# Kernel tuning notes

Measured on AMD Instinct MI355X. Metric: run time of the kernel, lower is better.

Reference implementation:

```python
import jax, jax.numpy as jnp
import numpy as np

B, S, H = 2, 2048, 2048
NH, HD = 16, 128
I = 8192
EPS = float(np.finfo(np.float32).eps)  # torch RMSNorm default eps=None -> dtype eps


def rmsnorm(x, w):
    var = jnp.mean(jnp.square(x), axis=-1, keepdims=True)
    return x * jax.lax.rsqrt(var + EPS) * w


def setup_inputs() -> dict:
    key = jax.random.key(0)
    ks = jax.random.split(key, 8)
    s = 0.02
    return {
        "hidden_states": jax.random.normal(ks[0], (B, S, H), jnp.float32),
        "Wq": jax.random.normal(ks[1], (H, H), jnp.float32) * s,
        "Wk": jax.random.normal(ks[2], (H, H), jnp.float32) * s,
        "Wv": jax.random.normal(ks[3], (H, H), jnp.float32) * s,
        "Wo": jax.random.normal(ks[4], (H, H), jnp.float32) * s,
        "Wg": jax.random.normal(ks[5], (I, H), jnp.float32) * s,
        "Wu": jax.random.normal(ks[6], (I, H), jnp.float32) * s,
        "Wd": jax.random.normal(ks[7], (H, I), jnp.float32) * s,
        "g_in": jnp.ones((H,), jnp.float32),
        "g_post": jnp.ones((H,), jnp.float32),
    }


def reference(hidden_states, Wq, Wk, Wv, Wo, Wg, Wu, Wd, g_in, g_post):
    residual = hidden_states
    x = rmsnorm(hidden_states, g_in)
    # projections: nn.Linear does x @ W.T
    q = (x @ Wq.T).reshape(B, S, NH, HD).transpose(0, 2, 1, 3)  # [B,NH,S,HD]
    k = (x @ Wk.T).reshape(B, S, NH, HD).transpose(0, 2, 1, 3)
    v = (x @ Wv.T).reshape(B, S, NH, HD).transpose(0, 2, 1, 3)
    scores = jnp.einsum("bhqd,bhkd->bhqk", q, k) / jnp.sqrt(jnp.float32(HD))
    attn = jax.nn.softmax(scores, axis=-1)
    out = jnp.einsum("bhqk,bhkd->bhqd", attn, v)
    out = out.transpose(0, 2, 1, 3).reshape(B, S, H)
    hidden_states = residual + out @ Wo.T
    residual = hidden_states
    x = rmsnorm(hidden_states, g_post)
    mlp = (jax.nn.silu(x @ Wg.T) * (x @ Wu.T)) @ Wd.T
    return residual + mlp
```

## Files before the change

### kernel.cpp

```cpp
#include <hip/hip_runtime.h>

using u16 = unsigned short;
using u32 = unsigned int;

typedef __attribute__((ext_vector_type(8))) __bf16 bf16x8;
typedef __attribute__((ext_vector_type(4))) float f32x4;

__device__ __forceinline__ u16 f2bf(float f) {
  __bf16 h = (__bf16)f;
  return __builtin_bit_cast(u16, h);
}
__device__ __forceinline__ u32 pk2(float a, float b) {
  return (u32)f2bf(a) | ((u32)f2bf(b) << 16);
}
__device__ __forceinline__ float bf2f(u16 h) {
  return __uint_as_float(((u32)h) << 16);
}
__device__ __forceinline__ void gload16(const u16* g, u16* l) {
  __builtin_amdgcn_global_load_lds((const __attribute__((address_space(1))) void*)g,
                                   (__attribute__((address_space(3))) void*)l, 16, 0, 0);
}
__device__ __forceinline__ f32x4 mfma_bf16(bf16x8 a, bf16x8 b, f32x4 c) {
  return __builtin_amdgcn_mfma_f32_16x16x32_bf16(a, b, c, 0, 0, 0);
}

__global__ __launch_bounds__(256) void cvt_bf16(const float* __restrict__ in,
                                                u16* __restrict__ out, int n8) {
  int i = blockIdx.x * 256 + threadIdx.x;
  int stride = gridDim.x * 256;
  for (; i < n8; i += stride) {
    float4 a = ((const float4*)in)[(size_t)i * 2];
    float4 b = ((const float4*)in)[(size_t)i * 2 + 1];
    ((uint4*)out)[i] = make_uint4(pk2(a.x, a.y), pk2(a.z, a.w), pk2(b.x, b.y), pk2(b.z, b.w));
  }
}

struct CvtJobs {
  const float* in[7];
  u16* out[7];
  int n8[7];
};
__global__ __launch_bounds__(256) void cvt_all(CvtJobs c) {
  const int stride = gridDim.x * 256;
  const int base = blockIdx.x * 256 + threadIdx.x;
#pragma unroll
  for (int j = 0; j < 7; ++j) {
    const float* in = c.in[j];
    u16* out = c.out[j];
    const int n8 = c.n8[j];
    for (int i = base; i < n8; i += stride) {
      float4 a = ((const float4*)in)[(size_t)i * 2];
      float4 b = ((const float4*)in)[(size_t)i * 2 + 1];
      ((uint4*)out)[i] = make_uint4(pk2(a.x, a.y), pk2(a.z, a.w), pk2(b.x, b.y), pk2(b.z, b.w));
    }
  }
}

__global__ __launch_bounds__(256) void rmsnorm_bf16(const float* __restrict__ x,
                                                    const float* __restrict__ g,
                                                    u16* __restrict__ o) {
  const int row = blockIdx.x;
  const int tid = threadIdx.x;
  const float4* xr = (const float4*)(x + (size_t)row * 2048);
  float4 a = xr[tid * 2], b = xr[tid * 2 + 1];
  float s = a.x * a.x + a.y * a.y + a.z * a.z + a.w * a.w +
            b.x * b.x + b.y * b.y + b.z * b.z + b.w * b.w;
#pragma unroll
  for (int off = 1; off < 64; off <<= 1) s += __shfl_xor(s, off);
  __shared__ float red[4];
  if ((tid & 63) == 0) red[tid >> 6] = s;
  __syncthreads();
  s = red[0] + red[1] + red[2] + red[3];
  const float r = rsqrtf(s * (1.0f / 2048.0f) + 1.1920929e-07f);
  const float4* gr = (const float4*)g;
  float4 ga = gr[tid * 2], gb = gr[tid * 2 + 1];
  ((uint4*)(o + (size_t)row * 2048))[tid] =
      make_uint4(pk2(a.x * r * ga.x, a.y * r * ga.y), pk2(a.z * r * ga.z, a.w * r * ga.w),
                 pk2(b.x * r * gb.x, b.y * r * gb.y), pk2(b.z * r * gb.z, b.w * r * gb.w));
}

__global__ __launch_bounds__(512, 2) void gemmGU(const u16* __restrict__ A,
                                                 const u16* __restrict__ Bg,
                                                 const u16* __restrict__ Bu,
                                                 u16* __restrict__ Out,
                                                 int M, int N, int K) {
  alignas(16) __shared__ u16 lds[2 * 32768];
  const int tid = threadIdx.x;
  const int w = tid >> 6, lane = tid & 63;
  const int lo = lane & 15, hi = lane >> 4;
  const int nbm = M >> 8, nbx = N >> 7;
  const int RM = nbm >> 1, RN = nbx >> 2;
  const int xcd = blockIdx.x & 7, bidx = blockIdx.x >> 3;
  const int bm = ((xcd >> 2) * RM + bidx / RN) << 8;
  const int bn = ((xcd & 3) * RN + bidx % RN) << 7;
  const int wm = w >> 1, wn = w & 1;

  const int rw = (hi ^ ((lo >> 1) & 3)) * 8;
  const int arow0 = wm * 64 + lo, brow0 = wn * 64 + lo;

  const int srow = tid >> 2;
  const int scol = ((tid & 3) ^ ((tid >> 3) & 3)) * 8;
  const u16* Ab = A + (size_t)(bm + srow) * K + scol;
  const u16* Bgb = Bg + (size_t)(bn + srow) * K + scol;
  const u16* Bub = Bu + (size_t)(bn + srow) * K + scol;

  f32x4 gacc[4][4] = {}, uacc[4][4] = {};
  bf16x8 af[4], bf[4];

#define AOFF(par, kh) ((par)*32768 + (kh)*8192)
#define BGOFF(par, kh) ((par)*32768 + 16384 + (kh)*4096)
#define BUOFF(par, kh) ((par)*32768 + 24576 + (kh)*4096)
#define STG_A(par, kh, kt)                                                  \
  {                                                                         \
    gload16(Ab + (kt) + (kh)*32, &lds[AOFF(par, kh) + tid * 8]);            \
    gload16(Ab + (size_t)128 * K + (kt) + (kh)*32,                          \
            &lds[AOFF(par, kh) + 4096 + tid * 8]);                          \
  }
#define STG_B(par, kh, kt)                                                  \
  {                                                                         \
    gload16(Bgb + (kt) + (kh)*32, &lds[BGOFF(par, kh) + tid * 8]);          \
    gload16(Bub + (kt) + (kh)*32, &lds[BUOFF(par, kh) + tid * 8]);          \
  }
#define PHASE_SYNC()                                   \
  __builtin_amdgcn_s_barrier();                        \
  asm volatile("s_waitcnt lgkmcnt(0)" ::: "memory");   \
  __builtin_amdgcn_sched_barrier(0);
#define MFMA16(ACC)                                                         \
  __builtin_amdgcn_s_setprio(1);                                            \
  _Pragma("unroll") for (int m_ = 0; m_ < 4; ++m_)                          \
      _Pragma("unroll") for (int n_ = 0; n_ < 4; ++n_)                      \
          ACC[m_][n_] = mfma_bf16(af[m_], bf[n_], ACC[m_][n_]);             \
  __builtin_amdgcn_s_setprio(0);

  STG_A(0, 0, 0); STG_B(0, 0, 0); STG_A(0, 1, 0); STG_B(0, 1, 0);
  asm volatile("s_waitcnt vmcnt(0)" ::: "memory");
  __builtin_amdgcn_s_barrier();

  const int NT = K >> 6;
  for (int t = 0; t < NT; ++t) {
    const int par = t & 1, np = par ^ 1;
    const int ktn = (t + 1) << 6;
    const bool pre = (t + 1 < NT);

#pragma unroll
    for (int n = 0; n < 4; ++n)
      bf[n] = *(const bf16x8*)(&lds[BGOFF(par, 0)] + (brow0 + n * 16) * 32 + rw);
#pragma unroll
    for (int m = 0; m < 4; ++m)
      af[m] = *(const bf16x8*)(&lds[AOFF(par, 0)] + (arow0 + m * 16) * 32 + rw);
    if (pre) STG_A(np, 0, ktn);
    PHASE_SYNC();
    MFMA16(gacc);

#pragma unroll
    for (int n = 0; n < 4; ++n)
      bf[n] = *(const bf16x8*)(&lds[BUOFF(par, 0)] + (brow0 + n * 16) * 32 + rw);
    if (pre) STG_B(np, 0, ktn);
    if (pre) { asm volatile("s_waitcnt vmcnt(4)" ::: "memory"); }
    else     { asm volatile("s_waitcnt vmcnt(0)" ::: "memory"); }
    PHASE_SYNC();
    MFMA16(uacc);

#pragma unroll
    for (int n = 0; n < 4; ++n)
      bf[n] = *(const bf16x8*)(&lds[BGOFF(par, 1)] + (brow0 + n * 16) * 32 + rw);
#pragma unroll
    for (int m = 0; m < 4; ++m)
      af[m] = *(const bf16x8*)(&lds[AOFF(par, 1)] + (arow0 + m * 16) * 32 + rw);
    if (pre) STG_A(np, 1, ktn);
    PHASE_SYNC();
    MFMA16(gacc);

#pragma unroll
    for (int n = 0; n < 4; ++n)
      bf[n] = *(const bf16x8*)(&lds[BUOFF(par, 1)] + (brow0 + n * 16) * 32 + rw);
    if (pre) STG_B(np, 1, ktn);
    if (pre) { asm volatile("s_waitcnt vmcnt(4)" ::: "memory"); }
    PHASE_SYNC();
    MFMA16(uacc);
  }
#undef AOFF
#undef BGOFF
#undef BUOFF
#undef STG_A
#undef STG_B
#undef PHASE_SYNC
#undef MFMA16

#pragma unroll
  for (int m = 0; m < 4; ++m) {
    const int gr = bm + wm * 64 + m * 16 + hi * 4;
#pragma unroll
    for (int n = 0; n < 4; ++n) {
      const int gc = bn + wn * 64 + n * 16 + lo;
#pragma unroll
      for (int r = 0; r < 4; ++r) {
        float g = gacc[m][n][r];
        float s = g / (1.f + __expf(-g));
        Out[(size_t)(gr + r) * N + gc] = f2bf(s * uacc[m][n][r]);
      }
    }
  }
}

template <int EPI>
__global__ __launch_bounds__(512, 1) void gemm3b(const u16* __restrict__ A,
                                                 const u16* __restrict__ B,
                                                 u16* Cb, float* Cf,
                                                 const float* __restrict__ Res,
                                                 int M, int N, int K, int lda) {
  constexpr int BUF = 24576;
  alignas(16) __shared__ u16 lds[3 * BUF];
  const int tid = threadIdx.x;
  const int w = tid >> 6, lane = tid & 63;
  const int lo = lane & 15, hi = lane >> 4;

  const int nbm = M >> 8, nbx = N >> 7;
  const int RM = nbm >> 1, RN = nbx >> 2;
  const int xcd = blockIdx.x & 7, idx = blockIdx.x >> 3;
  const int bm = ((xcd >> 2) * RM + idx / RN) << 8;
  const int bn = ((xcd & 3) * RN + idx % RN) << 7;

  const int wm = w >> 1, wn = w & 1;
  const int scol = ((tid & 7) ^ ((tid >> 3) & 7)) * 8;
  const u16* Ag = A + (size_t)(bm + (tid >> 3)) * lda + scol;
  const u16* Bg = B + (size_t)(bn + (tid >> 3)) * K + scol;

  f32x4 acc[4][4] = {};

#define STG(b, kt)                                                                    \
  {                                                                                   \
    _Pragma("unroll") for (int c = 0; c < 4; ++c)                                     \
        gload16(Ag + (size_t)(c * 64) * lda + (kt), &lds[(b)*BUF + c * 4096 + tid * 8]); \
    _Pragma("unroll") for (int c = 0; c < 2; ++c)                                     \
        gload16(Bg + (size_t)(c * 64) * K + (kt), &lds[(b)*BUF + 16384 + c * 4096 + tid * 8]); \
  }

  const int NT = K >> 6;
  STG(0, 0);
  STG(1, 64);

  int cur = 0;
  for (int T = 0; T < NT; ++T) {
    if (T + 1 < NT) {
      asm volatile("s_waitcnt vmcnt(6)" ::: "memory");
    } else {
      asm volatile("s_waitcnt vmcnt(0)" ::: "memory");
    }
    __builtin_amdgcn_s_barrier();
    __builtin_amdgcn_sched_barrier(0);

    const u16* LA = &lds[cur * BUF];
    const u16* LB = LA + 16384;
    bf16x8 af[4][2], bf[4][2];
#pragma unroll
    for (int ks = 0; ks < 2; ++ks) {
#pragma unroll
      for (int m = 0; m < 4; ++m)
        af[m][ks] = *(const bf16x8*)(LA + (wm * 64 + m * 16 + lo) * 64 +
                                     ((ks * 4 + hi) ^ (lo & 7)) * 8);
#pragma unroll
      for (int n = 0; n < 4; ++n)
        bf[n][ks] = *(const bf16x8*)(LB + (wn * 64 + n * 16 + lo) * 64 +
                                     ((ks * 4 + hi) ^ (lo & 7)) * 8);
    }
    if (T + 2 < NT) {
      const int nb = (cur + 2) % 3;
      STG(nb, (T + 2) << 6);
    }
    __builtin_amdgcn_s_setprio(1);
#pragma unroll
    for (int ks = 0; ks < 2; ++ks)
#pragma unroll
      for (int m = 0; m < 4; ++m)
#pragma unroll
        for (int n = 0; n < 4; ++n) acc[m][n] = mfma_bf16(af[m][ks], bf[n][ks], acc[m][n]);
    __builtin_amdgcn_s_setprio(0);
    cur = (cur + 1) % 3;
  }
#undef STG

#pragma unroll
  for (int m = 0; m < 4; ++m) {
    const int gr = bm + wm * 64 + m * 16 + hi * 4;
#pragma unroll
    for (int n = 0; n < 4; ++n) {
      const int gc = bn + wn * 64 + n * 16 + lo;
#pragma unroll
      for (int r = 0; r < 4; ++r) {
        const size_t idx2 = (size_t)(gr + r) * N + gc;
        if constexpr (EPI == 1) {
          Cf[idx2] = Res[idx2] + acc[m][n][r];
        } else if constexpr (EPI == 2) {
          float g = bf2f(Cb[idx2]);
          float s = g / (1.f + __expf(-g));
          Cb[idx2] = f2bf(s * acc[m][n][r]);
        } else {
          Cb[idx2] = f2bf(acc[m][n][r]);
        }
      }
    }
  }
}

template <int EPI>
__global__ __launch_bounds__(256) void gemm_bt(const u16* __restrict__ A,
                                               const float* __restrict__ B,
                                               u16* Cb, float* Cf, const float* Res,
                                               int M, int N, int K) {
  alignas(16) __shared__ u16 As[128 * 32];
  alignas(16) __shared__ u16 Bs[128 * 32];
  const int tid = threadIdx.x;
  const int w = tid >> 6, lane = tid & 63;
  const int lo = lane & 15, hi = lane >> 4;
  const int bm = blockIdx.y * 128, bn = blockIdx.x * 128;
  const int wr = (w >> 1) * 64, wc = (w & 1) * 64;
  f32x4 acc[4][4] = {};
  const int r0 = tid >> 2, kc0 = (tid & 3) * 8;
  const u16* a0 = A + (size_t)(bm + r0) * K + kc0;
  const u16* a1 = A + (size_t)(bm + 64 + r0) * K + kc0;
  const float* b0 = B + (size_t)(bn + r0) * K + kc0;
  const float* b1 = B + (size_t)(bn + 64 + r0) * K + kc0;
  u16* asd0 = &As[(size_t)tid * 8];
  u16* asd1 = &As[(size_t)(tid + 256) * 8];
  u16* bsd0 = &Bs[(size_t)tid * 8];
  u16* bsd1 = &Bs[(size_t)(tid + 256) * 8];
  for (int kt = 0; kt < K; kt += 32) {
    gload16(a0 + kt, asd0);
    gload16(a1 + kt, asd1);
    float4 x0 = *(const float4*)(b0 + kt);
    float4 x1 = *(const float4*)(b0 + kt + 4);
    float4 y0 = *(const float4*)(b1 + kt);
    float4 y1 = *(const float4*)(b1 + kt + 4);
    *(uint4*)bsd0 = make_uint4(pk2(x0.x, x0.y), pk2(x0.z, x0.w), pk2(x1.x, x1.y), pk2(x1.z, x1.w));
    *(uint4*)bsd1 = make_uint4(pk2(y0.x, y0.y), pk2(y0.z, y0.w), pk2(y1.x, y1.y), pk2(y1.z, y1.w));
    __syncthreads();
    bf16x8 af[4], bfr[4];
#pragma unroll
    for (int i = 0; i < 4; ++i) {
      af[i] = *(const bf16x8*)(&As[(wr + i * 16 + lo) * 32 + hi * 8]);
      bfr[i] = *(const bf16x8*)(&Bs[(wc + i * 16 + lo) * 32 + hi * 8]);
    }
#pragma unroll
    for (int i = 0; i < 4; ++i)
#pragma unroll
      for (int j = 0; j < 4; ++j) acc[i][j] = mfma_bf16(af[i], bfr[j], acc[i][j]);
    __syncthreads();
  }
#pragma unroll
  for (int i = 0; i < 4; ++i) {
    const int gr = bm + wr + i * 16 + hi * 4;
#pragma unroll
    for (int j = 0; j < 4; ++j) {
      const int gc = bn + wc + j * 16 + lo;
#pragma unroll
      for (int r = 0; r < 4; ++r) {
        const size_t idx = (size_t)(gr + r) * N + gc;
        if constexpr (EPI == 1) {
          Cf[idx] = Res[idx] + acc[i][j][r];
        } else if constexpr (EPI == 2) {
          float g = bf2f(Cb[idx]);
          float s = g / (1.f + __expf(-g));
          Cb[idx] = f2bf(s * acc[i][j][r]);
        } else {
          Cb[idx] = f2bf(acc[i][j][r]);
        }
      }
    }
  }
}

__global__ __launch_bounds__(256) void transpose_v(const u16* __restrict__ v,
                                                   u16* __restrict__ vt, int ldv) {
  __shared__ u16 t[32][33];
  const int bh = blockIdx.z, b = bh >> 4, h = bh & 15;
  const int s0 = blockIdx.x * 32, d0 = blockIdx.y * 32;
  const int tx = threadIdx.x, ty = threadIdx.y;
#pragma unroll
  for (int i = 0; i < 4; ++i)
    t[ty + i * 8][tx] = v[(size_t)(b * 2048 + s0 + ty + i * 8) * ldv + h * 128 + d0 + tx];
  __syncthreads();
#pragma unroll
  for (int i = 0; i < 4; ++i)
    vt[(size_t)(bh * 128 + d0 + ty + i * 8) * 2048 + s0 + tx] = t[tx][ty + i * 8];
}

__global__ __launch_bounds__(512) void attn_fwd3(const u16* __restrict__ q,
                                                 const u16* __restrict__ k,
                                                 const u16* __restrict__ vt,
                                                 u16* o, int ldq) {
  constexpr int S = 2048;
  alignas(16) __shared__ u16 Ks[2][64 * 128];
  alignas(16) __shared__ u16 Vs[2][128 * 64];
  alignas(16) __shared__ u16 plds[8][16 * 68];
  const int bh = blockIdx.y, b = bh >> 4, h = bh & 15;
  const int tid = threadIdx.x, w = tid >> 6, lane = tid & 63;
  const int lo = lane & 15, hi = lane >> 4;
  const int qr = blockIdx.x * 128 + w * 16;
  u16* pl = &plds[w][0];

  bf16x8 qf[4];
  const u16* qb = q + (size_t)(b * S + qr + lo) * ldq + h * 128 + hi * 8;
#pragma unroll
  for (int ks = 0; ks < 4; ++ks) qf[ks] = *(const bf16x8*)(qb + ks * 32);

  f32x4 oacc[8] = {};
  f32x4 lp = {0.f, 0.f, 0.f, 0.f};

  const u16* kb = k + (size_t)(b * S) * ldq + h * 128;
  const u16* vb = vt + (size_t)bh * 128 * S;

  const int kcs = ((tid & 15) ^ ((tid >> 4) & 7)) * 8;
  const int vcs = ((tid & 7) ^ ((tid >> 3) & 7)) * 8;
  const u16* kgs = kb + (size_t)(tid >> 4) * ldq + kcs;
  const u16* vgs = vb + (size_t)(tid >> 3) * S + vcs;

  int cur = 0;
#pragma unroll
  for (int c = 0; c < 2; ++c) gload16(kgs + (size_t)(c * 32) * ldq, &Ks[0][c * 4096 + tid * 8]);
#pragma unroll
  for (int c = 0; c < 2; ++c) gload16(vgs + (size_t)(c * 64) * S, &Vs[0][c * 4096 + tid * 8]);
  __syncthreads();

  const int swq = (lo & 7) << 4;
  constexpr float SCL = 0.12752956f;

  for (int kv = 0; kv < S; kv += 64) {
    if (kv + 64 < S) {
      const int nb = cur ^ 1;
#pragma unroll
      for (int c = 0; c < 2; ++c)
        gload16(kgs + (size_t)(kv + 64 + c * 32) * ldq, &Ks[nb][c * 4096 + tid * 8]);
#pragma unroll
      for (int c = 0; c < 2; ++c)
        gload16(vgs + (size_t)(c * 64) * S + kv + 64, &Vs[nb][c * 4096 + tid * 8]);
    }
    const u16* Kc = &Ks[cur][0];
    const u16* Vc = &Vs[cur][0];

    f32x4 sacc[4] = {};
    __builtin_amdgcn_s_setprio(1);
#pragma unroll
    for (int ks = 0; ks < 4; ++ks)
#pragma unroll
      for (int n = 0; n < 4; ++n) {
        bf16x8 kf = *(const bf16x8*)(Kc + (n * 16 + lo) * 128 + (((ks * 64 + hi * 16) ^ swq) >> 1));
        sacc[n] = mfma_bf16(qf[ks], kf, sacc[n]);
      }
    __builtin_amdgcn_s_setprio(0);

    f32x4 p[4];
#pragma unroll
    for (int n = 0; n < 4; ++n)
#pragma unroll
      for (int r = 0; r < 4; ++r) p[n][r] = exp2f(sacc[n][r] * SCL);
#pragma unroll
    for (int r = 0; r < 4; ++r)
      lp[r] += (p[0][r] + p[1][r]) + (p[2][r] + p[3][r]);

#pragma unroll
    for (int n = 0; n < 4; ++n)
#pragma unroll
      for (int r = 0; r < 4; ++r)
        pl[(hi * 4 + r) * 68 + n * 16 + lo] = f2bf(p[n][r]);
    asm volatile("s_waitcnt lgkmcnt(0)" ::: "memory");
    bf16x8 pf0 = *(const bf16x8*)(pl + lo * 68 + hi * 8);
    bf16x8 pf1 = *(const bf16x8*)(pl + lo * 68 + 32 + hi * 8);

    __builtin_amdgcn_s_setprio(1);
#pragma unroll
    for (int f = 0; f < 8; ++f) {
      const int row = f * 16 + lo;
      bf16x8 vf0 = *(const bf16x8*)(Vc + row * 64 + (((hi * 16) ^ swq) >> 1));
      bf16x8 vf1 = *(const bf16x8*)(Vc + row * 64 + (((64 + hi * 16) ^ swq) >> 1));
      oacc[f] = mfma_bf16(pf0, vf0, oacc[f]);
      oacc[f] = mfma_bf16(pf1, vf1, oacc[f]);
    }
    __builtin_amdgcn_s_setprio(0);

    __syncthreads();
    cur ^= 1;
  }

  float l[4];
#pragma unroll
  for (int r = 0; r < 4; ++r) l[r] = lp[r];
#pragma unroll
  for (int off = 1; off < 16; off <<= 1)
#pragma unroll
    for (int r = 0; r < 4; ++r) l[r] += __shfl_xor(l[r], off);

  u16* ob = o + (size_t)(b * S + qr) * ldq + h * 128;
#pragma unroll
  for (int f = 0; f < 8; ++f)
#pragma unroll
    for (int r = 0; r < 4; ++r)
      ob[(size_t)(hi * 4 + r) * ldq + f * 16 + lo] = f2bf(oacc[f][r] / l[r]);
}

extern "C" void kernel_launch(void* const* d_in, const int* in_sizes, int n_in,
                              void* d_out, int out_size, void* d_ws, size_t ws_size,
                              hipStream_t stream) {
  constexpr int B = 2, S = 2048, H = 2048, NH = 16, I = 8192;
  constexpr int M = B * S;

  const float* hs = (const float*)d_in[0];
  const float* Wq = (const float*)d_in[1];
  const float* Wk = (const float*)d_in[2];
  const float* Wv = (const float*)d_in[3];
  const float* Wo = (const float*)d_in[4];
  const float* Wg = (const float*)d_in[5];
  const float* Wu = (const float*)d_in[6];
  const float* Wd = (const float*)d_in[7];
  const float* g_in = (const float*)d_in[8];
  const float* g_post = (const float*)d_in[9];
  float* out = (float*)d_out;

  constexpr size_t SZ_HH = (size_t)H * H * 2;
  constexpr size_t SZ_IH = (size_t)I * H * 2;
  constexpr size_t SZ_MH = (size_t)M * H * 2;
  constexpr size_t NEED_ALL = 5 * SZ_MH + 3 * SZ_HH + SZ_HH + 3 * SZ_IH;
  constexpr size_t NEED_FUSED = SZ_MH + 3 * SZ_MH + SZ_MH + 2 * SZ_IH;
  constexpr size_t NEED_BASE = SZ_MH + 3 * SZ_MH + SZ_MH + SZ_IH;

  if (ws_size >= NEED_ALL) {
    char* p = (char*)d_ws;
    u16* x_b = (u16*)p;    p += SZ_MH;
    u16* qkv_b = (u16*)p;  p += 3 * SZ_MH;
    u16* vt_b = (u16*)p;   p += SZ_MH;
    u16* wqkv = (u16*)p;   p += 3 * SZ_HH;
    u16* wo_b = (u16*)p;   p += SZ_HH;
    u16* wg_b = (u16*)p;   p += SZ_IH;
    u16* wu_b = (u16*)p;   p += SZ_IH;
    u16* wd_b = (u16*)p;   p += SZ_IH;
    u16* gate_b = qkv_b;

    rmsnorm_bf16<<<M, 256, 0, stream>>>(hs, g_in, x_b);

    CvtJobs cj;
    cj.in[0] = Wq;  cj.out[0] = wqkv;                     cj.n8[0] = H * H / 8;
    cj.in[1] = Wk;  cj.out[1] = wqkv + (size_t)H * H;     cj.n8[1] = H * H / 8;
    cj.in[2] = Wv;  cj.out[2] = wqkv + (size_t)2 * H * H; cj.n8[2] = H * H / 8;
    cj.in[3] = Wo;  cj.out[3] = wo_b;                     cj.n8[3] = H * H / 8;
    cj.in[4] = Wg;  cj.out[4] = wg_b;                     cj.n8[4] = I * H / 8;
    cj.in[5] = Wu;  cj.out[5] = wu_b;                     cj.n8[5] = I * H / 8;
    cj.in[6] = Wd;  cj.out[6] = wd_b;                     cj.n8[6] = I * H / 8;
    cvt_all<<<2048, 256, 0, stream>>>(cj);

    gemm3b<0><<<(M / 256) * (3 * H / 128), 512, 0, stream>>>(
        x_b, wqkv, qkv_b, nullptr, nullptr, M, 3 * H, H, H);

    transpose_v<<<dim3(S / 32, 128 / 32, B * NH), dim3(32, 8), 0, stream>>>(
        qkv_b + 2 * H, vt_b, 3 * H);
    attn_fwd3<<<dim3(S / 128, B * NH), 512, 0, stream>>>(qkv_b, qkv_b + H, vt_b, qkv_b, 3 * H);

    gemm3b<1><<<(M / 256) * (H / 128), 512, 0, stream>>>(
        qkv_b, wo_b, nullptr, out, hs, M, H, H, 3 * H);

    rmsnorm_bf16<<<M, 256, 0, stream>>>(out, g_post, x_b);

    gemmGU<<<(M / 256) * (I / 128), 512, 0, stream>>>(x_b, wg_b, wu_b, gate_b, M, I, H);

    gemm3b<1><<<(M / 256) * (H / 128), 512, 0, stream>>>(
        gate_b, wd_b, nullptr, out, out, M, H, I, I);
    return;
  }

  if (ws_size >= NEED_BASE) {
    char* p = (char*)d_ws;
    u16* x_b = (u16*)p;    p += SZ_MH;
    u16* qkv_b = (u16*)p;  p += 3 * SZ_MH;
    u16* vt_b = (u16*)p;   p += SZ_MH;
    u16* wsc = (u16*)p;    p += SZ_IH;
    u16* gate_b = qkv_b;
    const bool fused = ws_size >= NEED_FUSED;
    u16* wu_b = fused ? (u16*)p : nullptr;

    rmsnorm_bf16<<<M, 256, 0, stream>>>(hs, g_in, x_b);

    cvt_bf16<<<1024, 256, 0, stream>>>(Wq, wsc, H * H / 8);
    cvt_bf16<<<1024, 256, 0, stream>>>(Wk, wsc + (size_t)H * H, H * H / 8);
    cvt_bf16<<<1024, 256, 0, stream>>>(Wv, wsc + (size_t)2 * H * H, H * H / 8);
    gemm3b<0><<<(M / 256) * (3 * H / 128), 512, 0, stream>>>(
        x_b, wsc, qkv_b, nullptr, nullptr, M, 3 * H, H, H);

    transpose_v<<<dim3(S / 32, 128 / 32, B * NH), dim3(32, 8), 0, stream>>>(
        qkv_b + 2 * H, vt_b, 3 * H);
    attn_fwd3<<<dim3(S / 128, B * NH), 512, 0, stream>>>(qkv_b, qkv_b + H, vt_b, qkv_b, 3 * H);

    cvt_bf16<<<1024, 256, 0, stream>>>(Wo, wsc, H * H / 8);
    gemm3b<1><<<(M / 256) * (H / 128), 512, 0, stream>>>(
        qkv_b, wsc, nullptr, out, hs, M, H, H, 3 * H);

    rmsnorm_bf16<<<M, 256, 0, stream>>>(out, g_post, x_b);

    if (fused) {
      cvt_bf16<<<1024, 256, 0, stream>>>(Wg, wsc, I * H / 8);
      cvt_bf16<<<1024, 256, 0, stream>>>(Wu, wu_b, I * H / 8);
      gemmGU<<<(M / 256) * (I / 128), 512, 0, stream>>>(x_b, wsc, wu_b, gate_b, M, I, H);
    } else {
      cvt_bf16<<<1024, 256, 0, stream>>>(Wg, wsc, I * H / 8);
      gemm3b<0><<<(M / 256) * (I / 128), 512, 0, stream>>>(
          x_b, wsc, gate_b, nullptr, nullptr, M, I, H, H);
      cvt_bf16<<<1024, 256, 0, stream>>>(Wu, wsc, I * H / 8);
      gemm3b<2><<<(M / 256) * (I / 128), 512, 0, stream>>>(
          x_b, wsc, gate_b, nullptr, nullptr, M, I, H, H);
    }
    cvt_bf16<<<1024, 256, 0, stream>>>(Wd, wsc, I * H / 8);
    gemm3b<1><<<(M / 256) * (H / 128), 512, 0, stream>>>(
        gate_b, wsc, nullptr, out, out, M, H, I, I);
    return;
  }

  constexpr int MC = 2048;
  char* p = (char*)d_ws;
  u16* x_b = (u16*)p;   p += SZ_MH;
  u16* q_b = (u16*)p;   p += SZ_MH;
  u16* k_b = (u16*)p;   p += SZ_MH;
  u16* v_b = (u16*)p;   p += SZ_MH;
  u16* vt_b = (u16*)p;  p += SZ_MH;
  u16* g_mlp = k_b;

  rmsnorm_bf16<<<M, 256, 0, stream>>>(hs, g_in, x_b);
  const dim3 gHH(H / 128, M / 128);
  gemm_bt<0><<<gHH, 256, 0, stream>>>(x_b, Wq, q_b, nullptr, nullptr, M, H, H);
  gemm_bt<0><<<gHH, 256, 0, stream>>>(x_b, Wk, k_b, nullptr, nullptr, M, H, H);
  gemm_bt<0><<<gHH, 256, 0, stream>>>(x_b, Wv, v_b, nullptr, nullptr, M, H, H);
  transpose_v<<<dim3(S / 32, 128 / 32, B * NH), dim3(32, 8), 0, stream>>>(v_b, vt_b, H);
  attn_fwd3<<<dim3(S / 128, B * NH), 512, 0, stream>>>(q_b, k_b, vt_b, q_b, H);
  gemm_bt<1><<<gHH, 256, 0, stream>>>(q_b, Wo, nullptr, out, hs, M, H, H);
  rmsnorm_bf16<<<M, 256, 0, stream>>>(out, g_post, x_b);
  const dim3 gIH(I / 128, MC / 128), gHI(H / 128, MC / 128);
  for (int mc = 0; mc < M / MC; ++mc) {
    const u16* xc = x_b + (size_t)mc * MC * H;
    float* oc = out + (size_t)mc * MC * H;
    gemm_bt<0><<<gIH, 256, 0, stream>>>(xc, Wg, g_mlp, nullptr, nullptr, MC, I, H);
    gemm_bt<2><<<gIH, 256, 0, stream>>>(xc, Wu, g_mlp, nullptr, nullptr, MC, I, H);
    gemm_bt<1><<<gHI, 256, 0, stream>>>(g_mlp, Wd, nullptr, oc, oc, MC, H, I);
  }
}
```

Measured before the change: 782.7 us.

## Switch gemmGU and gemm3b to 32x32x16 bf16 MFMA tiles

Replaces the 16x16x32 MFMA instruction with the 32x32x16 variant in the fused gate/up GEMM and the generic triple-buffered GEMM. Each wave now covers its 64x64 tile as a 2x2 grid of 32x32 blocks, with new swizzled LDS fragment addressing and remapped epilogue rows. This is meant to cut the LDS fragment reads per MFMA and the instruction count while raising arithmetic intensity per register fragment. gemmGU's launch bound drops from 2 blocks to 1 block per CU, which loosens the register cap but may lower occupancy.

```diff
diff --git a/kernel.cpp b/kernel.cpp
--- a/kernel.cpp
+++ b/kernel.cpp
@@ -5,6 +5,7 @@
 
 typedef __attribute__((ext_vector_type(8))) __bf16 bf16x8;
 typedef __attribute__((ext_vector_type(4))) float f32x4;
+typedef __attribute__((ext_vector_type(16))) float f32x16;
 
 __device__ __forceinline__ u16 f2bf(float f) {
   __bf16 h = (__bf16)f;
@@ -22,6 +23,9 @@
 }
 __device__ __forceinline__ f32x4 mfma_bf16(bf16x8 a, bf16x8 b, f32x4 c) {
   return __builtin_amdgcn_mfma_f32_16x16x32_bf16(a, b, c, 0, 0, 0);
+}
+__device__ __forceinline__ f32x16 mfma32(bf16x8 a, bf16x8 b, f32x16 c) {
+  return __builtin_amdgcn_mfma_f32_32x32x16_bf16(a, b, c, 0, 0, 0);
 }
 
 __global__ __launch_bounds__(256) void cvt_bf16(const float* __restrict__ in,
@@ -79,7 +83,7 @@
                  pk2(b.x * r * gb.x, b.y * r * gb.y), pk2(b.z * r * gb.z, b.w * r * gb.w));
 }
 
-__global__ __launch_bounds__(512, 2) void gemmGU(const u16* __restrict__ A,
+__global__ __launch_bounds__(512, 1) void gemmGU(const u16* __restrict__ A,
                                                  const u16* __restrict__ Bg,
                                                  const u16* __restrict__ Bu,
                                                  u16* __restrict__ Out,
@@ -87,7 +91,7 @@
   alignas(16) __shared__ u16 lds[2 * 32768];
   const int tid = threadIdx.x;
   const int w = tid >> 6, lane = tid & 63;
-  const int lo = lane & 15, hi = lane >> 4;
+  const int l31 = lane & 31, lh = lane >> 5;
   const int nbm = M >> 8, nbx = N >> 7;
   const int RM = nbm >> 1, RN = nbx >> 2;
   const int xcd = blockIdx.x & 7, bidx = blockIdx.x >> 3;
@@ -95,8 +99,10 @@
   const int bn = ((xcd & 3) * RN + bidx % RN) << 7;
   const int wm = w >> 1, wn = w & 1;
 
-  const int rw = (hi ^ ((lo >> 1) & 3)) * 8;
-  const int arow0 = wm * 64 + lo, brow0 = wn * 64 + lo;
+  const int keyA = (l31 >> 1) & 3;
+  const int aw0 = ((lh ^ keyA)) * 8;
+  const int arow = (wm * 64 + l31) * 32;
+  const int brow = (wn * 64 + l31) * 32;
 
   const int srow = tid >> 2;
   const int scol = ((tid & 3) ^ ((tid >> 3) & 3)) * 8;
@@ -104,8 +110,8 @@
   const u16* Bgb = Bg + (size_t)(bn + srow) * K + scol;
   const u16* Bub = Bu + (size_t)(bn + srow) * K + scol;
 
-  f32x4 gacc[4][4] = {}, uacc[4][4] = {};
-  bf16x8 af[4], bf[4];
+  f32x16 gacc[2][2] = {}, uacc[2][2] = {};
+  bf16x8 af[2][2], bf[2][2];
 
 #define AOFF(par, kh) ((par)*32768 + (kh)*8192)
 #define BGOFF(par, kh) ((par)*32768 + 16384 + (kh)*4096)
@@ -125,11 +131,22 @@
   __builtin_amdgcn_s_barrier();                        \
   asm volatile("s_waitcnt lgkmcnt(0)" ::: "memory");   \
   __builtin_amdgcn_sched_barrier(0);
-#define MFMA16(ACC)                                                         \
-  __builtin_amdgcn_s_setprio(1);                                            \
-  _Pragma("unroll") for (int m_ = 0; m_ < 4; ++m_)                          \
-      _Pragma("unroll") for (int n_ = 0; n_ < 4; ++n_)                      \
-          ACC[m_][n_] = mfma_bf16(af[m_], bf[n_], ACC[m_][n_]);             \
+#define LD_A(slot)                                                             \
+  _Pragma("unroll") for (int mb = 0; mb < 2; ++mb)                             \
+      _Pragma("unroll") for (int kq = 0; kq < 2; ++kq)                         \
+          af[mb][kq] = *(const bf16x8*)(&lds[(slot) + arow + mb * 1024 +       \
+                                             (aw0 ^ (kq * 16))]);
+#define LD_B(slot)                                                             \
+  _Pragma("unroll") for (int nb = 0; nb < 2; ++nb)                             \
+      _Pragma("unroll") for (int kq = 0; kq < 2; ++kq)                         \
+          bf[nb][kq] = *(const bf16x8*)(&lds[(slot) + brow + nb * 1024 +       \
+                                             (aw0 ^ (kq * 16))]);
+#define MFMA8(ACC)                                                             \
+  __builtin_amdgcn_s_setprio(1);                                               \
+  _Pragma("unroll") for (int kq = 0; kq < 2; ++kq)                             \
+      _Pragma("unroll") for (int mb = 0; mb < 2; ++mb)                         \
+          _Pragma("unroll") for (int nb = 0; nb < 2; ++nb)                     \
+              ACC[mb][nb] = mfma32(af[mb][kq], bf[nb][kq], ACC[mb][nb]);       \
   __builtin_amdgcn_s_setprio(0);
 
   STG_A(0, 0, 0); STG_B(0, 0, 0); STG_A(0, 1, 0); STG_B(0, 1, 0);
@@ -142,42 +159,30 @@
     const int ktn = (t + 1) << 6;
     const bool pre = (t + 1 < NT);
 
-#pragma unroll
-    for (int n = 0; n < 4; ++n)
-      bf[n] = *(const bf16x8*)(&lds[BGOFF(par, 0)] + (brow0 + n * 16) * 32 + rw);
-#pragma unroll
-    for (int m = 0; m < 4; ++m)
-      af[m] = *(const bf16x8*)(&lds[AOFF(par, 0)] + (arow0 + m * 16) * 32 + rw);
+    LD_B(BGOFF(par, 0));
+    LD_A(AOFF(par, 0));
     if (pre) STG_A(np, 0, ktn);
     PHASE_SYNC();
-    MFMA16(gacc);
-
-#pragma unroll
-    for (int n = 0; n < 4; ++n)
-      bf[n] = *(const bf16x8*)(&lds[BUOFF(par, 0)] + (brow0 + n * 16) * 32 + rw);
+    MFMA8(gacc);
+
+    LD_B(BUOFF(par, 0));
     if (pre) STG_B(np, 0, ktn);
     if (pre) { asm volatile("s_waitcnt vmcnt(4)" ::: "memory"); }
     else     { asm volatile("s_waitcnt vmcnt(0)" ::: "memory"); }
     PHASE_SYNC();
-    MFMA16(uacc);
-
-#pragma unroll
-    for (int n = 0; n < 4; ++n)
-      bf[n] = *(const bf16x8*)(&lds[BGOFF(par, 1)] + (brow0 + n * 16) * 32 + rw);
-#pragma unroll
-    for (int m = 0; m < 4; ++m)
-      af[m] = *(const bf16x8*)(&lds[AOFF(par, 1)] + (arow0 + m * 16) * 32 + rw);
+    MFMA8(uacc);
+
+    LD_B(BGOFF(par, 1));
+    LD_A(AOFF(par, 1));
     if (pre) STG_A(np, 1, ktn);
     PHASE_SYNC();
-    MFMA16(gacc);
-
-#pragma unroll
-    for (int n = 0; n < 4; ++n)
-      bf[n] = *(const bf16x8*)(&lds[BUOFF(par, 1)] + (brow0 + n * 16) * 32 + rw);
+    MFMA8(gacc);
+
+    LD_B(BUOFF(par, 1));
     if (pre) STG_B(np, 1, ktn);
     if (pre) { asm volatile("s_waitcnt vmcnt(4)" ::: "memory"); }
     PHASE_SYNC();
-    MFMA16(uacc);
+    MFMA8(uacc);
   }
 #undef AOFF
 #undef BGOFF
@@ -185,22 +190,23 @@
 #undef STG_A
 #undef STG_B
 #undef PHASE_SYNC
-#undef MFMA16
-
-#pragma unroll
-  for (int m = 0; m < 4; ++m) {
-    const int gr = bm + wm * 64 + m * 16 + hi * 4;
-#pragma unroll
-    for (int n = 0; n < 4; ++n) {
-      const int gc = bn + wn * 64 + n * 16 + lo;
-#pragma unroll
-      for (int r = 0; r < 4; ++r) {
-        float g = gacc[m][n][r];
+#undef LD_A
+#undef LD_B
+#undef MFMA8
+
+#pragma unroll
+  for (int mb = 0; mb < 2; ++mb)
+#pragma unroll
+    for (int nb = 0; nb < 2; ++nb) {
+      const int gc = bn + wn * 64 + nb * 32 + l31;
+#pragma unroll
+      for (int reg = 0; reg < 16; ++reg) {
+        const int gr = bm + wm * 64 + mb * 32 + (reg & 3) + 8 * (reg >> 2) + 4 * lh;
+        float g = gacc[mb][nb][reg];
         float s = g / (1.f + __expf(-g));
-        Out[(size_t)(gr + r) * N + gc] = f2bf(s * uacc[m][n][r]);
+        Out[(size_t)gr * N + gc] = f2bf(s * uacc[mb][nb][reg]);
       }
     }
-  }
 }
 
 template <int EPI>
@@ -213,7 +219,7 @@
   alignas(16) __shared__ u16 lds[3 * BUF];
   const int tid = threadIdx.x;
   const int w = tid >> 6, lane = tid & 63;
-  const int lo = lane & 15, hi = lane >> 4;
+  const int l31 = lane & 31, lh = lane >> 5;
 
   const int nbm = M >> 8, nbx = N >> 7;
   const int RM = nbm >> 1, RN = nbx >> 2;
@@ -222,11 +228,16 @@
   const int bn = ((xcd & 3) * RN + idx % RN) << 7;
 
   const int wm = w >> 1, wn = w & 1;
+  const int key7 = l31 & 7;
+  const int aw0 = (lh ^ key7) * 8;
+  const int arow = (wm * 64 + l31) * 64;
+  const int brow = (wn * 64 + l31) * 64;
+
   const int scol = ((tid & 7) ^ ((tid >> 3) & 7)) * 8;
   const u16* Ag = A + (size_t)(bm + (tid >> 3)) * lda + scol;
   const u16* Bg = B + (size_t)(bn + (tid >> 3)) * K + scol;
 
-  f32x4 acc[4][4] = {};
+  f32x16 acc[2][2] = {};
 
 #define STG(b, kt)                                                                    \
   {                                                                                   \
@@ -252,55 +263,54 @@
 
     const u16* LA = &lds[cur * BUF];
     const u16* LB = LA + 16384;
-    bf16x8 af[4][2], bf[4][2];
-#pragma unroll
-    for (int ks = 0; ks < 2; ++ks) {
-#pragma unroll
-      for (int m = 0; m < 4; ++m)
-        af[m][ks] = *(const bf16x8*)(LA + (wm * 64 + m * 16 + lo) * 64 +
-                                     ((ks * 4 + hi) ^ (lo & 7)) * 8);
-#pragma unroll
-      for (int n = 0; n < 4; ++n)
-        bf[n][ks] = *(const bf16x8*)(LB + (wn * 64 + n * 16 + lo) * 64 +
-                                     ((ks * 4 + hi) ^ (lo & 7)) * 8);
-    }
+    bf16x8 af[2][4], bf[2][4];
+#pragma unroll
+    for (int mb = 0; mb < 2; ++mb)
+#pragma unroll
+      for (int kq = 0; kq < 4; ++kq)
+        af[mb][kq] = *(const bf16x8*)(LA + arow + mb * 2048 + (aw0 ^ (kq * 16)));
+#pragma unroll
+    for (int nb = 0; nb < 2; ++nb)
+#pragma unroll
+      for (int kq = 0; kq < 4; ++kq)
+        bf[nb][kq] = *(const bf16x8*)(LB + brow + nb * 2048 + (aw0 ^ (kq * 16)));
     if (T + 2 < NT) {
-      const int nb = (cur + 2) % 3;
-      STG(nb, (T + 2) << 6);
+      const int nb2 = (cur + 2) % 3;
+      STG(nb2, (T + 2) << 6);
     }
     __builtin_amdgcn_s_setprio(1);
 #pragma unroll
-    for (int ks = 0; ks < 2; ++ks)
-#pragma unroll
-      for (int m = 0; m < 4; ++m)
-#pragma unroll
-        for (int n = 0; n < 4; ++n) acc[m][n] = mfma_bf16(af[m][ks], bf[n][ks], acc[m][n]);
+    for (int kq = 0; kq < 4; ++kq)
+#pragma unroll
+      for (int mb = 0; mb < 2; ++mb)
+#pragma unroll
+        for (int nb = 0; nb < 2; ++nb)
+          acc[mb][nb] = mfma32(af[mb][kq], bf[nb][kq], acc[mb][nb]);
     __builtin_amdgcn_s_setprio(0);
     cur = (cur + 1) % 3;
   }
 #undef STG
 
 #pragma unroll
-  for (int m = 0; m < 4; ++m) {
-    const int gr = bm + wm * 64 + m * 16 + hi * 4;
-#pragma unroll
-    for (int n = 0; n < 4; ++n) {
-      const int gc = bn + wn * 64 + n * 16 + lo;
-#pragma unroll
-      for (int r = 0; r < 4; ++r) {
-        const size_t idx2 = (size_t)(gr + r) * N + gc;
+  for (int mb = 0; mb < 2; ++mb)
+#pragma unroll
+    for (int nb = 0; nb < 2; ++nb) {
+      const int gc = bn + wn * 64 + nb * 32 + l31;
+#pragma unroll
+      for (int reg = 0; reg < 16; ++reg) {
+        const int gr = bm + wm * 64 + mb * 32 + (reg & 3) + 8 * (reg >> 2) + 4 * lh;
+        const size_t idx2 = (size_t)gr * N + gc;
         if constexpr (EPI == 1) {
-          Cf[idx2] = Res[idx2] + acc[m][n][r];
+          Cf[idx2] = Res[idx2] + acc[mb][nb][reg];
         } else if constexpr (EPI == 2) {
           float g = bf2f(Cb[idx2]);
           float s = g / (1.f + __expf(-g));
-          Cb[idx2] = f2bf(s * acc[m][n][r]);
+          Cb[idx2] = f2bf(s * acc[mb][nb][reg]);
         } else {
-          Cb[idx2] = f2bf(acc[m][n][r]);
+          Cb[idx2] = f2bf(acc[mb][nb][reg]);
         }
       }
     }
-  }
 }
 
 template <int EPI>
```

Result: slower. 838.8 us (+7.2%).
